# Kernel tuning notes

Hardware: AMD Instinct MI355X
Metric: run time of the kernel (lower is better)

Reference implementation:

```python
import jax, jax.numpy as jnp
import numpy as np

DIM = 768
HEADS = 12
WS = 8       # window_size
EPS = 1e-5   # torch LayerNorm eps


def _ln(x, g, b):
    m = jnp.mean(x, axis=-1, keepdims=True)
    v = jnp.var(x, axis=-1, keepdims=True)
    return (x - m) / jnp.sqrt(v + EPS) * g + b


def _attention(xw, qkv_w, proj_w, proj_b):
    # xw: (Bw, N, C) with N = WS*WS
    Bw, N, C = xw.shape
    D = C // HEADS
    scale = D ** -0.5
    # torch does x.reshape(3, B, N, C//3): a flat row-major split, identical in jax
    x3 = xw.reshape(3, Bw, N, C // 3)
    def tile(t):  # cat((t,t,t)) then reshape(B,N,C), exactly as torch
        return jnp.concatenate([t, t, t], axis=0).reshape(Bw, N, C)
    red, green, blue = tile(x3[0]), tile(x3[1]), tile(x3[2])
    # qkv Linear has no bias (qkv_bias=False); only k,v of Red and q of Green/Blue
    # are used, and q_green + q_blue == (green+blue) @ Wq^T
    Wq, Wk, Wv = qkv_w[:C], qkv_w[C:2 * C], qkv_w[2 * C:]
    def heads(t):  # (Bw,N,C) -> (Bw,H,N,D)
        return t.reshape(Bw, N, HEADS, D).transpose(0, 2, 1, 3)
    q = heads((green + blue) @ Wq.T)
    k = heads(red @ Wk.T)
    v = heads(red @ Wv.T)
    attn = jax.nn.softmax(jnp.einsum('bhnd,bhmd->bhnm', q, k) * scale, axis=-1)
    out = jnp.einsum('bhnm,bhmd->bhnd', attn, v).transpose(0, 2, 1, 3).reshape(Bw, N, C)
    return out @ proj_w.T + proj_b


def setup_inputs() -> dict:
    key = jax.random.key(0)
    ks = jax.random.split(key, 6)
    B, H, W, C = 4, 128, 128, DIM
    def p(k, shape):
        return jax.random.normal(k, shape, jnp.float32) * 0.02
    return {
        'x': jax.random.normal(ks[0], (B, H * W, C), jnp.float32),
        'norm1_g': jnp.ones((C,), jnp.float32),
        'norm1_b': jnp.zeros((C,), jnp.float32),
        'norm2_g': jnp.ones((C,), jnp.float32),
        'norm2_b': jnp.zeros((C,), jnp.float32),
        'qkv_w': p(ks[1], (3 * C, C)),
        'proj_w': p(ks[2], (C, C)),
        'proj_b': jnp.zeros((C,), jnp.float32),
        'fc1_w': p(ks[3], (1, C)),   # Mlp hidden_features hardcoded to 1 in source
        'fc1_b': jnp.zeros((1,), jnp.float32),
        'fc2_w': p(ks[4], (C, 1)),
        'fc2_b': jnp.zeros((C,), jnp.float32),
        'h': 128,
        'w': 128,
    }


def reference(x, norm1_g, norm1_b, norm2_g, norm2_b, qkv_w, proj_w, proj_b,
              fc1_w, fc1_b, fc2_w, fc2_b, h, w):
    B, L, C = x.shape
    xn = _ln(x, norm1_g, norm1_b).reshape(B, h, w, C)
    # window_partition: (B,H,W,C) -> (nW*B, WS*WS, C)
    xw = xn.reshape(B, h // WS, WS, w // WS, WS, C)
    xw = xw.transpose(0, 1, 3, 2, 4, 5).reshape(-1, WS * WS, C)
    a = _attention(xw, qkv_w, proj_w, proj_b)
    a = _ln(a, norm2_g, norm2_b)
    # NOTE: source has NO residual connections; output is mlp(norm2(attn(...)))
    hdn = jax.nn.gelu(a @ fc1_w.T + fc1_b, approximate=False)  # torch GELU = exact erf
    m = hdn @ fc2_w.T + fc2_b
    return m.reshape(B, h * w, C)
```

## Files before the change

kernel.cpp:

```cpp
#include <hip/hip_runtime.h>
#include <hip/hip_bf16.h>
#include <stdint.h>
#include <stddef.h>

typedef __bf16 bf16;
typedef __bf16 bf16x4 __attribute__((ext_vector_type(4)));
typedef __bf16 bf16x8 __attribute__((ext_vector_type(8)));
typedef float  f32x4  __attribute__((ext_vector_type(4)));

__device__ __forceinline__ void async16(const void* src, void* dst) {
    __builtin_amdgcn_global_load_lds(
        (__attribute__((address_space(1))) void*)(void*)(src),
        (__attribute__((address_space(3))) void*)(dst),
        16, 0, 0);
}

#define MEMFENCE asm volatile("" ::: "memory")

__device__ __forceinline__ void barrier_f() {
    MEMFENCE;
    __builtin_amdgcn_s_barrier();
    MEMFENCE;
}

__global__ __launch_bounds__(256)
void f2b(const float* __restrict__ src, bf16* __restrict__ dst, int n)
{
    const int i = (blockIdx.x * 256 + threadIdx.x) * 4;
    if (i < n) {
        f32x4 c = *(const f32x4*)(src + i);
        bf16x4 o;
        #pragma unroll
        for (int q = 0; q < 4; ++q) o[q] = (bf16)c[q];
        *(bf16x4*)(dst + i) = o;
    }
}

__global__ __launch_bounds__(256)
void ln1_win(const float* __restrict__ x, const float* __restrict__ g,
             const float* __restrict__ b, bf16* __restrict__ Y)
{
    const int row  = blockIdx.x * 4 + (threadIdx.x >> 6);
    const int lane = threadIdx.x & 63;
    const float* xr = x + (size_t)row * 768;
    float v[12];
    float sum = 0.f, ssq = 0.f;
    #pragma unroll
    for (int j = 0; j < 3; ++j) {
        f32x4 c = *(const f32x4*)(xr + j * 256 + lane * 4);
        #pragma unroll
        for (int q = 0; q < 4; ++q) {
            float f = c[q];
            v[j * 4 + q] = f; sum += f; ssq += f * f;
        }
    }
    #pragma unroll
    for (int d = 1; d < 64; d <<= 1) {
        sum += __shfl_xor(sum, d, 64);
        ssq += __shfl_xor(ssq, d, 64);
    }
    const float mean = sum * (1.f / 768.f);
    const float rstd = rsqrtf(ssq * (1.f / 768.f) - mean * mean + 1e-5f);
    const int bb = row >> 14;
    const int l  = row & 16383;
    const int hy = l >> 7, wx = l & 127;
    const int m  = ((bb * 256 + (hy >> 3) * 16 + (wx >> 3)) << 6)
                 + ((hy & 7) << 3) + (wx & 7);
    bf16* yr = Y + (size_t)m * 768;
    #pragma unroll
    for (int j = 0; j < 3; ++j) {
        const int c0 = j * 256 + lane * 4;
        f32x4 gg = *(const f32x4*)(g + c0);
        f32x4 bv = *(const f32x4*)(b + c0);
        bf16x4 ov;
        #pragma unroll
        for (int q = 0; q < 4; ++q)
            ov[q] = (bf16)((v[j * 4 + q] - mean) * rstd * gg[q] + bv[q]);
        *(bf16x4*)(yr + c0) = ov;
    }
}

__global__ __launch_bounds__(256)
void gsum(const bf16* __restrict__ Y, bf16* __restrict__ G, int Smod)
{
    const int i = (blockIdx.x * 256 + threadIdx.x) * 8;
    if (i < Smod) {
        bf16x8 a = *(const bf16x8*)(Y + Smod + i);
        bf16x8 c = *(const bf16x8*)(Y + 2 * Smod + i);
        bf16x8 r;
        #pragma unroll
        for (int q = 0; q < 8; ++q) r[q] = (bf16)((float)a[q] + (float)c[q]);
        *(bf16x8*)(G + i) = r;
    }
}

template<int AMODE, bool BIAS>
__global__ __launch_bounds__(512, 2)
void gemm8p(const bf16* __restrict__ A, const bf16* __restrict__ Yg,
            const bf16* __restrict__ Gb, const bf16* __restrict__ Bm,
            const float* __restrict__ bias, bf16* __restrict__ Cm,
            int K, int ldc, int Smod, int nb_n)
{
    __shared__ bf16 lds[2 * 32768];

    const int per    = gridDim.x >> 3;
    const int mchunk = per / nb_n;
    const int xcd    = blockIdx.x & 7;
    const int slot_b = blockIdx.x >> 3;
    const int mbase  = (xcd * mchunk + slot_b / nb_n) * 256;
    const int nbase  = (slot_b % nb_n) * 256;

    const int tid  = threadIdx.x;
    const int lane = tid & 63;
    const int w    = tid >> 6;
    const int quad = lane >> 4;
    const int l16  = lane & 15;
    const int wm   = (w >> 2) * 128;
    const int wn   = (w & 3) * 64;

    const bf16* Asrc = (AMODE == 1) ? ((nbase < 768) ? Gb : Yg) : A;
    const int nt = K >> 6;

    auto stage = [&](int kt, int X, int ks) {
        bf16* base = lds + (kt & 1) * 32768 + X * 16384 + ks * 8192;
        const int kb = kt * 64 + ks * 32;
        #pragma unroll
        for (int c = 0; c < 2; ++c) {
            const int idx = tid + c * 512;
            const int r   = idx >> 2;
            const int q   = (idx & 3) ^ ((r >> 1) & 3);
            const bf16* s;
            if (X == 0) {
                if (AMODE == 1) {
                    int f = (mbase + r) * 768 + kb + q * 8;
                    if (f >= 2 * Smod) f -= 2 * Smod;
                    else if (f >= Smod) f -= Smod;
                    s = Asrc + f;
                } else {
                    s = Asrc + (size_t)(mbase + r) * K + kb + q * 8;
                }
            } else {
                s = Bm + (size_t)(nbase + r) * K + kb + q * 8;
            }
            async16(s, base + idx * 8);
        }
    };

    auto readA = [&](bf16x8* af, int kt, int ks) {
        const bf16* base = lds + (kt & 1) * 32768 + ks * 8192;
        #pragma unroll
        for (int i = 0; i < 8; ++i) {
            const int r = wm + 16 * i + l16;
            const int q = quad ^ ((r >> 1) & 3);
            af[i] = *(const bf16x8*)(base + r * 32 + q * 8);
        }
    };
    auto readB = [&](bf16x8* bfr, int kt, int ks, int nh) {
        const bf16* base = lds + (kt & 1) * 32768 + 16384 + ks * 8192;
        #pragma unroll
        for (int j = 0; j < 2; ++j) {
            const int r = wn + nh * 32 + 16 * j + l16;
            const int q = quad ^ ((r >> 1) & 3);
            bfr[j] = *(const bf16x8*)(base + r * 32 + q * 8);
        }
    };

    const f32x4 zero = {0.f, 0.f, 0.f, 0.f};
    f32x4 acc[8][4];
    #pragma unroll
    for (int i = 0; i < 8; ++i)
        #pragma unroll
        for (int j = 0; j < 4; ++j) acc[i][j] = zero;

    auto mma16 = [&](const bf16x8* af, const bf16x8* bfr, int nh) {
        __builtin_amdgcn_s_setprio(1);
        #pragma unroll
        for (int i = 0; i < 8; ++i)
            #pragma unroll
            for (int jj = 0; jj < 2; ++jj)
                acc[i][nh * 2 + jj] = __builtin_amdgcn_mfma_f32_16x16x32_bf16(
                    af[i], bfr[jj], acc[i][nh * 2 + jj], 0, 0, 0);
        __builtin_amdgcn_s_setprio(0);
    };

    stage(0, 0, 0); stage(0, 1, 0); stage(0, 0, 1); stage(0, 1, 1);
    if (nt > 1) { stage(1, 0, 0); stage(1, 1, 0); }
    asm volatile("s_waitcnt vmcnt(8)" ::: "memory");
    barrier_f();

    bf16x8 af[8], bfr[2];
    for (int kt = 0; kt < nt; ++kt) {
        readA(af, kt, 0);
        readB(bfr, kt, 0, 0);
        if (kt + 1 < nt) stage(kt + 1, 0, 1);
        barrier_f();
        asm volatile("s_waitcnt lgkmcnt(0)" ::: "memory");
        mma16(af, bfr, 0);
        barrier_f();

        readB(bfr, kt, 0, 1);
        if (kt + 1 < nt) stage(kt + 1, 1, 1);
        if (kt < nt - 2) asm volatile("s_waitcnt vmcnt(6)" ::: "memory");
        else             asm volatile("s_waitcnt vmcnt(0)" ::: "memory");
        barrier_f();
        asm volatile("s_waitcnt lgkmcnt(0)" ::: "memory");
        mma16(af, bfr, 1);
        barrier_f();

        readA(af, kt, 1);
        readB(bfr, kt, 1, 0);
        if (kt + 2 < nt) stage(kt + 2, 0, 0);
        barrier_f();
        asm volatile("s_waitcnt lgkmcnt(0)" ::: "memory");
        mma16(af, bfr, 0);
        barrier_f();

        readB(bfr, kt, 1, 1);
        if (kt + 2 < nt) stage(kt + 2, 1, 0);
        if (kt < nt - 2) asm volatile("s_waitcnt vmcnt(6)" ::: "memory");
        else             asm volatile("s_waitcnt vmcnt(0)" ::: "memory");
        barrier_f();
        asm volatile("s_waitcnt lgkmcnt(0)" ::: "memory");
        mma16(af, bfr, 1);
        barrier_f();
    }

    #pragma unroll
    for (int i = 0; i < 8; ++i) {
        const int row0 = mbase + wm + 16 * i + quad * 4;
        #pragma unroll
        for (int j = 0; j < 4; ++j) {
            const int col = nbase + wn + 16 * j + l16;
            float bv = 0.f;
            if (BIAS) bv = bias[col];
            #pragma unroll
            for (int r = 0; r < 4; ++r)
                Cm[(size_t)(row0 + r) * ldc + col] = (bf16)(acc[i][j][r] + bv);
        }
    }
}

__global__ __launch_bounds__(64)
void attn_win(const bf16* __restrict__ QKV, bf16* __restrict__ AOut)
{
    const int blk  = blockIdx.x;
    const int bw   = blk / 12;
    const int h    = blk % 12;
    const int lane = threadIdx.x;
    const int quad = lane >> 4;
    const int l16  = lane & 15;

    __shared__ bf16 Kt[64 * 64];
    __shared__ bf16 Vt[64 * 64];

    const size_t rowbase = (size_t)bw * 64;

    {
        const int rsub = lane >> 3;
        const int slot = lane & 7;
        #pragma unroll
        for (int t = 0; t < 8; ++t) {
            const int row = 8 * t + rsub;
            const int kcK = slot ^ (row & 7);
            async16(QKV + (rowbase + row) * 2304 + 768 + h * 64 + kcK * 8,
                    Kt + (8 * t) * 64);
            async16(QKV + (rowbase + row) * 2304 + 1536 + h * 64 + slot * 8,
                    Vt + (8 * t) * 64);
        }
    }

    bf16x8 qf[4][2];
    #pragma unroll
    for (int i = 0; i < 4; ++i)
        #pragma unroll
        for (int ks = 0; ks < 2; ++ks)
            qf[i][ks] = *(const bf16x8*)(QKV + (rowbase + 16 * i + l16) * 2304
                                         + h * 64 + ks * 32 + quad * 8);
    __syncthreads();

    const f32x4 zero = {0.f, 0.f, 0.f, 0.f};
    f32x4 s[4][4];
    #pragma unroll
    for (int i = 0; i < 4; ++i)
        #pragma unroll
        for (int j = 0; j < 4; ++j) s[i][j] = zero;

    #pragma unroll
    for (int ks = 0; ks < 2; ++ks) {
        bf16x8 kf[4];
        #pragma unroll
        for (int j = 0; j < 4; ++j) {
            const int row  = 16 * j + l16;
            const int slot = (ks * 4 + quad) ^ (row & 7);
            kf[j] = *(const bf16x8*)(Kt + row * 64 + slot * 8);
        }
        #pragma unroll
        for (int i = 0; i < 4; ++i)
            #pragma unroll
            for (int j = 0; j < 4; ++j)
                s[i][j] = __builtin_amdgcn_mfma_f32_16x16x32_bf16(
                    qf[i][ks], kf[j], s[i][j], 0, 0, 0);
    }

    float rrec[4][4];
    #pragma unroll
    for (int i = 0; i < 4; ++i) {
        #pragma unroll
        for (int r = 0; r < 4; ++r) {
            float mx = s[i][0][r];
            #pragma unroll
            for (int j = 1; j < 4; ++j) mx = fmaxf(mx, s[i][j][r]);
            #pragma unroll
            for (int d = 1; d < 16; d <<= 1) mx = fmaxf(mx, __shfl_xor(mx, d, 64));
            float sum = 0.f;
            #pragma unroll
            for (int j = 0; j < 4; ++j) {
                float p = __expf((s[i][j][r] - mx) * 0.125f);
                s[i][j][r] = p;
                sum += p;
            }
            #pragma unroll
            for (int d = 1; d < 16; d <<= 1) sum += __shfl_xor(sum, d, 64);
            rrec[i][r] = 1.f / sum;
        }
    }

    #pragma unroll
    for (int i = 0; i < 4; ++i)
        #pragma unroll
        for (int j = 0; j < 4; ++j)
            #pragma unroll
            for (int r = 0; r < 4; ++r) {
                const int row  = 16 * i + quad * 4 + r;
                const int col  = 16 * j + l16;
                const int slot = (col >> 3) ^ (row & 7);
                Kt[row * 64 + slot * 8 + (col & 7)] = (bf16)s[i][j][r];
            }
    __syncthreads();

    f32x4 o[4][4];
    #pragma unroll
    for (int i = 0; i < 4; ++i)
        #pragma unroll
        for (int j = 0; j < 4; ++j) o[i][j] = zero;

    #pragma unroll
    for (int ks = 0; ks < 2; ++ks) {
        bf16x8 pf[4], vf[4];
        #pragma unroll
        for (int i = 0; i < 4; ++i) {
            const int row  = 16 * i + l16;
            const int slot = (ks * 4 + quad) ^ (row & 7);
            pf[i] = *(const bf16x8*)(Kt + row * 64 + slot * 8);
        }
        #pragma unroll
        for (int j = 0; j < 4; ++j) {
            bf16x8 t;
            #pragma unroll
            for (int q = 0; q < 8; ++q)
                t[q] = Vt[(ks * 32 + quad * 8 + q) * 64 + 16 * j + l16];
            vf[j] = t;
        }
        #pragma unroll
        for (int i = 0; i < 4; ++i)
            #pragma unroll
            for (int j = 0; j < 4; ++j)
                o[i][j] = __builtin_amdgcn_mfma_f32_16x16x32_bf16(
                    pf[i], vf[j], o[i][j], 0, 0, 0);
    }

    #pragma unroll
    for (int i = 0; i < 4; ++i)
        #pragma unroll
        for (int j = 0; j < 4; ++j)
            #pragma unroll
            for (int r = 0; r < 4; ++r) {
                const size_t grow = rowbase + 16 * i + quad * 4 + r;
                const int col = h * 64 + 16 * j + l16;
                AOut[grow * 768 + col] = (bf16)(o[i][j][r] * rrec[i][r]);
            }
}

__global__ __launch_bounds__(256)
void final_fused(const bf16* __restrict__ P, const float* __restrict__ g2,
                 const float* __restrict__ b2, const float* __restrict__ fc1w,
                 const float* __restrict__ fc1b, const float* __restrict__ fc2w,
                 const float* __restrict__ fc2b, float* __restrict__ out)
{
    const int row  = blockIdx.x * 4 + (threadIdx.x >> 6);
    const int lane = threadIdx.x & 63;
    const bf16* pr = P + (size_t)row * 768;
    float v[12];
    float sum = 0.f, ssq = 0.f;
    #pragma unroll
    for (int j = 0; j < 3; ++j) {
        bf16x4 c = *(const bf16x4*)(pr + j * 256 + lane * 4);
        #pragma unroll
        for (int q = 0; q < 4; ++q) {
            float f = (float)c[q];
            v[j * 4 + q] = f; sum += f; ssq += f * f;
        }
    }
    #pragma unroll
    for (int d = 1; d < 64; d <<= 1) {
        sum += __shfl_xor(sum, d, 64);
        ssq += __shfl_xor(ssq, d, 64);
    }
    const float mean = sum * (1.f / 768.f);
    const float rstd = rsqrtf(ssq * (1.f / 768.f) - mean * mean + 1e-5f);
    float part = 0.f;
    #pragma unroll
    for (int j = 0; j < 3; ++j) {
        const int c0 = j * 256 + lane * 4;
        f32x4 gg = *(const f32x4*)(g2 + c0);
        f32x4 bb = *(const f32x4*)(b2 + c0);
        f32x4 f1 = *(const f32x4*)(fc1w + c0);
        #pragma unroll
        for (int q = 0; q < 4; ++q) {
            float ln = (v[j * 4 + q] - mean) * rstd * gg[q] + bb[q];
            part += ln * f1[q];
        }
    }
    #pragma unroll
    for (int d = 1; d < 64; d <<= 1) part += __shfl_xor(part, d, 64);
    const float sv = part + fc1b[0];
    const float ge = 0.5f * sv * (1.f + erff(sv * 0.70710678118654752f));
    float* orow = out + (size_t)row * 768;
    #pragma unroll
    for (int j = 0; j < 3; ++j) {
        const int c0 = j * 256 + lane * 4;
        f32x4 f2  = *(const f32x4*)(fc2w + c0);
        f32x4 b2v = *(const f32x4*)(fc2b + c0);
        f32x4 ov;
        #pragma unroll
        for (int q = 0; q < 4; ++q)
            ov[q] = ge * f2[q] + b2v[q];
        *(f32x4*)(orow + c0) = ov;
    }
}

extern "C" void kernel_launch(void* const* d_in, const int* in_sizes, int n_in,
                              void* d_out, int out_size, void* d_ws, size_t ws_size,
                              hipStream_t stream)
{
    const float* x     = (const float*)d_in[0];
    const float* n1g   = (const float*)d_in[1];
    const float* n1b   = (const float*)d_in[2];
    const float* n2g   = (const float*)d_in[3];
    const float* n2b   = (const float*)d_in[4];
    const float* qkvw  = (const float*)d_in[5];
    const float* projw = (const float*)d_in[6];
    const float* projb = (const float*)d_in[7];
    const float* fc1w  = (const float*)d_in[8];
    const float* fc1b  = (const float*)d_in[9];
    const float* fc2w  = (const float*)d_in[10];
    const float* fc2b  = (const float*)d_in[11];
    float* out = (float*)d_out;

    const int total = in_sizes[0];
    const int rows  = total / 768;
    const int Smod  = total / 3;
    const int Bw    = rows / 64;
    const int C     = 768;

    bf16* qkv     = (bf16*)d_ws;
    bf16* Ybuf    = qkv + (size_t)rows * 2304;
    bf16* qkvw_b  = Ybuf + (size_t)rows * 768;
    bf16* projw_b = qkvw_b + (size_t)3 * C * C;
    bf16* Pbuf    = qkv;
    bf16* Gb      = (bf16*)d_out;

    const int nqkvw  = 3 * C * C;
    const int nprojw = C * C;
    f2b<<<(nqkvw / 4 + 255) / 256, 256, 0, stream>>>(qkvw, qkvw_b, nqkvw);
    f2b<<<(nprojw / 4 + 255) / 256, 256, 0, stream>>>(projw, projw_b, nprojw);

    ln1_win<<<rows / 4, 256, 0, stream>>>(x, n1g, n1b, Ybuf);

    gsum<<<(Smod / 8 + 255) / 256, 256, 0, stream>>>(Ybuf, Gb, Smod);

    const int nbm = rows / 256;
    gemm8p<1, false><<<nbm * 9, 512, 0, stream>>>(
        nullptr, Ybuf, Gb, qkvw_b, nullptr, qkv, 768, 2304, Smod, 9);

    attn_win<<<Bw * 12, 64, 0, stream>>>(qkv, Ybuf);

    gemm8p<0, true><<<nbm * 3, 512, 0, stream>>>(
        Ybuf, nullptr, nullptr, projw_b, projb, Pbuf, 768, 768, 0, 3);

    final_fused<<<rows / 4, 256, 0, stream>>>(Pbuf, n2g, n2b, fc1w, fc1b,
                                              fc2w, fc2b, out);
}
```

Measured before the change: 867.6 us.

## Overlap LDS fragment reads with MFMA using double-buffered B registers in GEMM

Restructures the GEMM main loop so that LDS reads for the next sub-step are issued right after the current MFMA batch, using two B register sets. This drops the explicit lgkmcnt waits and halves the barriers per k-tile from eight to four. Global staging now issues A and B together per k-slice, and source addresses and swizzled LDS offsets are computed once outside the loop. The gain is less address math and barrier stalls, paid for with extra register pressure and a tighter reliance on the compiler's own waitcnt insertion for correctness.

```diff
diff --git a/kernel.cpp b/kernel.cpp
--- a/kernel.cpp
+++ b/kernel.cpp
@@ -121,48 +121,73 @@
     const bf16* Asrc = (AMODE == 1) ? ((nbase < 768) ? Gb : Yg) : A;
     const int nt = K >> 6;
 
-    auto stage = [&](int kt, int X, int ks) {
-        bf16* base = lds + (kt & 1) * 32768 + X * 16384 + ks * 8192;
+    const int r0 = tid >> 2, r1 = r0 + 128;
+    const int q0 = (tid & 3) ^ ((r0 >> 1) & 3);
+    const int q1 = (tid & 3) ^ ((r1 >> 1) & 3);
+    const int lo0 = tid * 8, lo1 = tid * 8 + 4096;
+
+    int f0A0 = 0, f0A1 = 0;
+    const bf16 *aP0 = nullptr, *aP1 = nullptr;
+    if (AMODE == 1) {
+        f0A0 = (mbase + r0) * 768 + q0 * 8;
+        if (f0A0 >= 2 * Smod) f0A0 -= 2 * Smod;
+        else if (f0A0 >= Smod) f0A0 -= Smod;
+        f0A1 = (mbase + r1) * 768 + q1 * 8;
+        if (f0A1 >= 2 * Smod) f0A1 -= 2 * Smod;
+        else if (f0A1 >= Smod) f0A1 -= Smod;
+    } else {
+        aP0 = A + (size_t)(mbase + r0) * K + q0 * 8;
+        aP1 = A + (size_t)(mbase + r1) * K + q1 * 8;
+    }
+    const bf16* bP0 = Bm + (size_t)(nbase + r0) * K + q0 * 8;
+    const bf16* bP1 = Bm + (size_t)(nbase + r1) * K + q1 * 8;
+
+    auto stageK = [&](int kt, int ks) {
         const int kb = kt * 64 + ks * 32;
-        #pragma unroll
-        for (int c = 0; c < 2; ++c) {
-            const int idx = tid + c * 512;
-            const int r   = idx >> 2;
-            const int q   = (idx & 3) ^ ((r >> 1) & 3);
-            const bf16* s;
-            if (X == 0) {
-                if (AMODE == 1) {
-                    int f = (mbase + r) * 768 + kb + q * 8;
-                    if (f >= 2 * Smod) f -= 2 * Smod;
-                    else if (f >= Smod) f -= Smod;
-                    s = Asrc + f;
-                } else {
-                    s = Asrc + (size_t)(mbase + r) * K + kb + q * 8;
-                }
-            } else {
-                s = Bm + (size_t)(nbase + r) * K + kb + q * 8;
-            }
-            async16(s, base + idx * 8);
-        }
+        bf16* dst = lds + (kt & 1) * 32768 + ks * 8192;
+        const bf16 *s0, *s1;
+        if (AMODE == 1) {
+            int f = f0A0 + kb; if (f >= Smod) f -= Smod;
+            int g = f0A1 + kb; if (g >= Smod) g -= Smod;
+            s0 = Asrc + f; s1 = Asrc + g;
+        } else {
+            s0 = aP0 + kb; s1 = aP1 + kb;
+        }
+        async16(s0, dst + lo0);
+        async16(s1, dst + lo1);
+        async16(bP0 + kb, dst + 16384 + lo0);
+        async16(bP1 + kb, dst + 16384 + lo1);
     };
 
-    auto readA = [&](bf16x8* af, int kt, int ks) {
-        const bf16* base = lds + (kt & 1) * 32768 + ks * 8192;
-        #pragma unroll
-        for (int i = 0; i < 8; ++i) {
-            const int r = wm + 16 * i + l16;
-            const int q = quad ^ ((r >> 1) & 3);
-            af[i] = *(const bf16x8*)(base + r * 32 + q * 8);
-        }
-    };
-    auto readB = [&](bf16x8* bfr, int kt, int ks, int nh) {
-        const bf16* base = lds + (kt & 1) * 32768 + 16384 + ks * 8192;
+    int aoff[8], boff[2][2];
+    #pragma unroll
+    for (int i = 0; i < 8; ++i) {
+        const int r = wm + 16 * i + l16;
+        aoff[i] = r * 32 + (quad ^ ((r >> 1) & 3)) * 8;
+    }
+    #pragma unroll
+    for (int nh = 0; nh < 2; ++nh)
         #pragma unroll
         for (int j = 0; j < 2; ++j) {
             const int r = wn + nh * 32 + 16 * j + l16;
-            const int q = quad ^ ((r >> 1) & 3);
-            bfr[j] = *(const bf16x8*)(base + r * 32 + q * 8);
-        }
+            boff[nh][j] = r * 32 + (quad ^ ((r >> 1) & 3)) * 8;
+        }
+
+    bf16x8 af[8], b0[2], b1[2];
+    auto readA = [&](int p, int ks) {
+        const bf16* base = lds + p + ks * 8192;
+        #pragma unroll
+        for (int i = 0; i < 8; ++i) af[i] = *(const bf16x8*)(base + aoff[i]);
+    };
+    auto readB0 = [&](int p, int ks, int nh) {
+        const bf16* base = lds + p + 16384 + ks * 8192;
+        #pragma unroll
+        for (int j = 0; j < 2; ++j) b0[j] = *(const bf16x8*)(base + boff[nh][j]);
+    };
+    auto readB1 = [&](int p, int ks, int nh) {
+        const bf16* base = lds + p + 16384 + ks * 8192;
+        #pragma unroll
+        for (int j = 0; j < 2; ++j) b1[j] = *(const bf16x8*)(base + boff[nh][j]);
     };
 
     const f32x4 zero = {0.f, 0.f, 0.f, 0.f};
@@ -172,57 +197,65 @@
         #pragma unroll
         for (int j = 0; j < 4; ++j) acc[i][j] = zero;
 
-    auto mma16 = [&](const bf16x8* af, const bf16x8* bfr, int nh) {
+    auto mma16 = [&](const bf16x8* bb, int ch) {
         __builtin_amdgcn_s_setprio(1);
         #pragma unroll
         for (int i = 0; i < 8; ++i)
             #pragma unroll
             for (int jj = 0; jj < 2; ++jj)
-                acc[i][nh * 2 + jj] = __builtin_amdgcn_mfma_f32_16x16x32_bf16(
-                    af[i], bfr[jj], acc[i][nh * 2 + jj], 0, 0, 0);
+                acc[i][ch * 2 + jj] = __builtin_amdgcn_mfma_f32_16x16x32_bf16(
+                    af[i], bb[jj], acc[i][ch * 2 + jj], 0, 0, 0);
         __builtin_amdgcn_s_setprio(0);
     };
 
-    stage(0, 0, 0); stage(0, 1, 0); stage(0, 0, 1); stage(0, 1, 1);
-    if (nt > 1) { stage(1, 0, 0); stage(1, 1, 0); }
-    asm volatile("s_waitcnt vmcnt(8)" ::: "memory");
+    stageK(0, 0); stageK(0, 1);
+    if (nt > 1) {
+        stageK(1, 0);
+        asm volatile("s_waitcnt vmcnt(8)" ::: "memory");
+    } else {
+        asm volatile("s_waitcnt vmcnt(4)" ::: "memory");
+    }
     barrier_f();
-
-    bf16x8 af[8], bfr[2];
+    readA(0, 0);
+    readB0(0, 0, 0);
+
     for (int kt = 0; kt < nt; ++kt) {
-        readA(af, kt, 0);
-        readB(bfr, kt, 0, 0);
-        if (kt + 1 < nt) stage(kt + 1, 0, 1);
+        const int p = (kt & 1) * 32768;
+
         barrier_f();
-        asm volatile("s_waitcnt lgkmcnt(0)" ::: "memory");
-        mma16(af, bfr, 0);
+        mma16(b0, 0);
+        readB1(p, 0, 1);
+        if (kt + 1 < nt) {
+            stageK(kt + 1, 1);
+            asm volatile("s_waitcnt vmcnt(8)" ::: "memory");
+        } else {
+            asm volatile("s_waitcnt vmcnt(0)" ::: "memory");
+        }
+
         barrier_f();
-
-        readB(bfr, kt, 0, 1);
-        if (kt + 1 < nt) stage(kt + 1, 1, 1);
-        if (kt < nt - 2) asm volatile("s_waitcnt vmcnt(6)" ::: "memory");
-        else             asm volatile("s_waitcnt vmcnt(0)" ::: "memory");
+        mma16(b1, 1);
+        readA(p, 1);
+        readB0(p, 1, 0);
+
         barrier_f();
-        asm volatile("s_waitcnt lgkmcnt(0)" ::: "memory");
-        mma16(af, bfr, 1);
+        mma16(b0, 0);
+        readB1(p, 1, 1);
+        if (kt + 2 < nt) {
+            stageK(kt + 2, 0);
+            asm volatile("s_waitcnt vmcnt(8)" ::: "memory");
+        } else if (kt + 1 < nt) {
+            asm volatile("s_waitcnt vmcnt(4)" ::: "memory");
+        } else {
+            asm volatile("s_waitcnt vmcnt(0)" ::: "memory");
+        }
+
         barrier_f();
-
-        readA(af, kt, 1);
-        readB(bfr, kt, 1, 0);
-        if (kt + 2 < nt) stage(kt + 2, 0, 0);
-        barrier_f();
-        asm volatile("s_waitcnt lgkmcnt(0)" ::: "memory");
-        mma16(af, bfr, 0);
-        barrier_f();
-
-        readB(bfr, kt, 1, 1);
-        if (kt + 2 < nt) stage(kt + 2, 1, 0);
-        if (kt < nt - 2) asm volatile("s_waitcnt vmcnt(6)" ::: "memory");
-        else             asm volatile("s_waitcnt vmcnt(0)" ::: "memory");
-        barrier_f();
-        asm volatile("s_waitcnt lgkmcnt(0)" ::: "memory");
-        mma16(af, bfr, 1);
-        barrier_f();
+        mma16(b1, 1);
+        if (kt + 1 < nt) {
+            const int pn = ((kt + 1) & 1) * 32768;
+            readA(pn, 0);
+            readB0(pn, 0, 0);
+        }
     }
 
     #pragma unroll
```

Result: no change. 858.6 us (-1.0%).

## Load GEMM B operand directly into registers and triple-buffer A in LDS

Applied to the files above, without the earlier changes.

The GEMM kernel no longer stages the weight (B) tile through LDS. Each lane loads its B fragments straight from global memory into registers, double-buffered across the two k-halves. The A tile moves to a three-stage LDS ring with one barrier per k-step instead of eight, and address offsets are precomputed outside the loop. This is meant to cut LDS traffic and barrier overhead, at the cost of uncoalesced-ish global B reads that rely on cache reuse across blocks, plus higher register pressure.

```diff
diff --git a/kernel.cpp b/kernel.cpp
--- a/kernel.cpp
+++ b/kernel.cpp
@@ -96,12 +96,12 @@
 
 template<int AMODE, bool BIAS>
 __global__ __launch_bounds__(512, 2)
-void gemm8p(const bf16* __restrict__ A, const bf16* __restrict__ Yg,
-            const bf16* __restrict__ Gb, const bf16* __restrict__ Bm,
-            const float* __restrict__ bias, bf16* __restrict__ Cm,
-            int K, int ldc, int Smod, int nb_n)
-{
-    __shared__ bf16 lds[2 * 32768];
+void gemm_bd(const bf16* __restrict__ A, const bf16* __restrict__ Yg,
+             const bf16* __restrict__ Gb, const bf16* __restrict__ Bm,
+             const float* __restrict__ bias, bf16* __restrict__ Cm,
+             int K, int ldc, int Smod, int nb_n)
+{
+    __shared__ bf16 lds[3 * 16384];
 
     const int per    = gridDim.x >> 3;
     const int mchunk = per / nb_n;
@@ -121,48 +121,63 @@
     const bf16* Asrc = (AMODE == 1) ? ((nbase < 768) ? Gb : Yg) : A;
     const int nt = K >> 6;
 
-    auto stage = [&](int kt, int X, int ks) {
-        bf16* base = lds + (kt & 1) * 32768 + X * 16384 + ks * 8192;
-        const int kb = kt * 64 + ks * 32;
-        #pragma unroll
-        for (int c = 0; c < 2; ++c) {
-            const int idx = tid + c * 512;
-            const int r   = idx >> 2;
-            const int q   = (idx & 3) ^ ((r >> 1) & 3);
-            const bf16* s;
-            if (X == 0) {
-                if (AMODE == 1) {
-                    int f = (mbase + r) * 768 + kb + q * 8;
-                    if (f >= 2 * Smod) f -= 2 * Smod;
-                    else if (f >= Smod) f -= Smod;
-                    s = Asrc + f;
-                } else {
-                    s = Asrc + (size_t)(mbase + r) * K + kb + q * 8;
-                }
+    const int r0 = tid >> 2;
+    const int cq = tid & 3;
+    const int q0 = cq ^ ((r0 >> 1) & 3);
+    int fA0 = 0, fA1 = 0;
+    const bf16 *aP0 = nullptr, *aP1 = nullptr;
+    if (AMODE == 1) {
+        fA0 = (mbase + r0) * 768 + q0 * 8;
+        if (fA0 >= 2 * Smod) fA0 -= 2 * Smod;
+        else if (fA0 >= Smod) fA0 -= Smod;
+        fA1 = (mbase + r0 + 128) * 768 + q0 * 8;
+        if (fA1 >= 2 * Smod) fA1 -= 2 * Smod;
+        else if (fA1 >= Smod) fA1 -= Smod;
+    } else {
+        aP0 = A + (size_t)(mbase + r0) * K + q0 * 8;
+        aP1 = A + (size_t)(mbase + r0 + 128) * K + q0 * 8;
+    }
+    const int ldst0 = tid * 8;
+    const int ldst1 = tid * 8 + 4096;
+
+    auto stageA = [&](int kt) {
+        bf16* dst = lds + (kt % 3) * 16384;
+        const int kb = kt * 64;
+        #pragma unroll
+        for (int ks = 0; ks < 2; ++ks) {
+            const int ko = kb + ks * 32;
+            const bf16 *s0, *s1;
+            if (AMODE == 1) {
+                int f = fA0 + ko; if (f >= Smod) f -= Smod;
+                int g = fA1 + ko; if (g >= Smod) g -= Smod;
+                s0 = Asrc + f; s1 = Asrc + g;
             } else {
-                s = Bm + (size_t)(nbase + r) * K + kb + q * 8;
+                s0 = aP0 + ko; s1 = aP1 + ko;
             }
-            async16(s, base + idx * 8);
+            async16(s0, dst + ks * 8192 + ldst0);
+            async16(s1, dst + ks * 8192 + ldst1);
         }
     };
 
-    auto readA = [&](bf16x8* af, int kt, int ks) {
-        const bf16* base = lds + (kt & 1) * 32768 + ks * 8192;
-        #pragma unroll
-        for (int i = 0; i < 8; ++i) {
-            const int r = wm + 16 * i + l16;
-            const int q = quad ^ ((r >> 1) & 3);
-            af[i] = *(const bf16x8*)(base + r * 32 + q * 8);
-        }
-    };
-    auto readB = [&](bf16x8* bfr, int kt, int ks, int nh) {
-        const bf16* base = lds + (kt & 1) * 32768 + 16384 + ks * 8192;
-        #pragma unroll
-        for (int j = 0; j < 2; ++j) {
-            const int r = wn + nh * 32 + 16 * j + l16;
-            const int q = quad ^ ((r >> 1) & 3);
-            bfr[j] = *(const bf16x8*)(base + r * 32 + q * 8);
-        }
+    int aoff[8];
+    #pragma unroll
+    for (int i = 0; i < 8; ++i) {
+        const int r = wm + 16 * i + l16;
+        aoff[i] = r * 32 + (quad ^ ((r >> 1) & 3)) * 8;
+    }
+
+    const bf16* bPtr[4];
+    #pragma unroll
+    for (int b = 0; b < 4; ++b) {
+        const int row = nbase + wn + 16 * b + l16;
+        bPtr[b] = Bm + (size_t)row * K + quad * 8;
+    }
+
+    bf16x8 af[8], Ba[4], Bb[4];
+    auto readA = [&](int kt, int ks) {
+        const bf16* base = lds + (kt % 3) * 16384 + ks * 8192;
+        #pragma unroll
+        for (int i = 0; i < 8; ++i) af[i] = *(const bf16x8*)(base + aoff[i]);
     };
 
     const f32x4 zero = {0.f, 0.f, 0.f, 0.f};
@@ -172,56 +187,51 @@
         #pragma unroll
         for (int j = 0; j < 4; ++j) acc[i][j] = zero;
 
-    auto mma16 = [&](const bf16x8* af, const bf16x8* bfr, int nh) {
+    auto mma32 = [&](const bf16x8* bb) {
         __builtin_amdgcn_s_setprio(1);
         #pragma unroll
         for (int i = 0; i < 8; ++i)
             #pragma unroll
-            for (int jj = 0; jj < 2; ++jj)
-                acc[i][nh * 2 + jj] = __builtin_amdgcn_mfma_f32_16x16x32_bf16(
-                    af[i], bfr[jj], acc[i][nh * 2 + jj], 0, 0, 0);
+            for (int b = 0; b < 4; ++b)
+                acc[i][b] = __builtin_amdgcn_mfma_f32_16x16x32_bf16(
+                    af[i], bb[b], acc[i][b], 0, 0, 0);
         __builtin_amdgcn_s_setprio(0);
     };
 
-    stage(0, 0, 0); stage(0, 1, 0); stage(0, 0, 1); stage(0, 1, 1);
-    if (nt > 1) { stage(1, 0, 0); stage(1, 1, 0); }
-    asm volatile("s_waitcnt vmcnt(8)" ::: "memory");
+    stageA(0);
+    MEMFENCE;
+    #pragma unroll
+    for (int b = 0; b < 4; ++b) Ba[b] = *(const bf16x8*)(bPtr[b]);
+    MEMFENCE;
+    if (nt > 1) stageA(1);
+    MEMFENCE;
+    asm volatile("s_waitcnt vmcnt(4)" ::: "memory");
     barrier_f();
 
-    bf16x8 af[8], bfr[2];
     for (int kt = 0; kt < nt; ++kt) {
-        readA(af, kt, 0);
-        readB(bfr, kt, 0, 0);
-        if (kt + 1 < nt) stage(kt + 1, 0, 1);
-        barrier_f();
-        asm volatile("s_waitcnt lgkmcnt(0)" ::: "memory");
-        mma16(af, bfr, 0);
-        barrier_f();
-
-        readB(bfr, kt, 0, 1);
-        if (kt + 1 < nt) stage(kt + 1, 1, 1);
-        if (kt < nt - 2) asm volatile("s_waitcnt vmcnt(6)" ::: "memory");
-        else             asm volatile("s_waitcnt vmcnt(0)" ::: "memory");
-        barrier_f();
-        asm volatile("s_waitcnt lgkmcnt(0)" ::: "memory");
-        mma16(af, bfr, 1);
-        barrier_f();
-
-        readA(af, kt, 1);
-        readB(bfr, kt, 1, 0);
-        if (kt + 2 < nt) stage(kt + 2, 0, 0);
-        barrier_f();
-        asm volatile("s_waitcnt lgkmcnt(0)" ::: "memory");
-        mma16(af, bfr, 0);
-        barrier_f();
-
-        readB(bfr, kt, 1, 1);
-        if (kt + 2 < nt) stage(kt + 2, 1, 0);
-        if (kt < nt - 2) asm volatile("s_waitcnt vmcnt(6)" ::: "memory");
-        else             asm volatile("s_waitcnt vmcnt(0)" ::: "memory");
-        barrier_f();
-        asm volatile("s_waitcnt lgkmcnt(0)" ::: "memory");
-        mma16(af, bfr, 1);
+        const int koff = kt * 64;
+
+        readA(kt, 0);
+        if (kt + 2 < nt) stageA(kt + 2);
+        MEMFENCE;
+        #pragma unroll
+        for (int b = 0; b < 4; ++b)
+            Bb[b] = *(const bf16x8*)(bPtr[b] + koff + 32);
+        MEMFENCE;
+
+        mma32(Ba);
+
+        readA(kt, 1);
+        if (kt + 1 < nt) {
+            #pragma unroll
+            for (int b = 0; b < 4; ++b)
+                Ba[b] = *(const bf16x8*)(bPtr[b] + koff + 64);
+        }
+        MEMFENCE;
+
+        mma32(Bb);
+
+        __builtin_amdgcn_sched_barrier(0);
         barrier_f();
     }
 
@@ -480,12 +490,12 @@
     gsum<<<(Smod / 8 + 255) / 256, 256, 0, stream>>>(Ybuf, Gb, Smod);
 
     const int nbm = rows / 256;
-    gemm8p<1, false><<<nbm * 9, 512, 0, stream>>>(
+    gemm_bd<1, false><<<nbm * 9, 512, 0, stream>>>(
         nullptr, Ybuf, Gb, qkvw_b, nullptr, qkv, 768, 2304, Smod, 9);
 
     attn_win<<<Bw * 12, 64, 0, stream>>>(qkv, Ybuf);
 
-    gemm8p<0, true><<<nbm * 3, 512, 0, stream>>>(
+    gemm_bd<0, true><<<nbm * 3, 512, 0, stream>>>(
         Ybuf, nullptr, nullptr, projw_b, projb, Pbuf, 768, 768, 0, 3);
 
     final_fused<<<rows / 4, 256, 0, stream>>>(Pbuf, n2g, n2b, fc1w, fc1b,
```

After: 941.4 us. 8.5% more time.
